# Optimization experiments

Hardware: AMD Instinct MI355X
Metric: run time of the kernel (lower is better)

## Reference

```python
import jax, jax.numpy as jnp
import numpy as np

B = 512
C = 256
HEADS = 16
DH = 16
SIGMA = 1e-4  # GaussianNoise(0.0001)
LEAK = 0.2


def _axial_attn(x, Wq, Wkv, Wo, bo, axis):
    # x: [B, 8, 4, 5, C]; attend along `axis`, folding other dims into batch.
    xm = jnp.moveaxis(x, axis, -2)                      # [..., T, C]
    q = xm @ Wq                                          # [..., T, C]
    kv = xm @ Wkv                                        # [..., T, 2C]
    k, v = kv[..., :C], kv[..., C:]
    hshape = q.shape[:-1] + (HEADS, DH)
    q = q.reshape(hshape)
    k = k.reshape(hshape)
    v = v.reshape(hshape)
    dots = jnp.einsum('...thd,...shd->...hts', q, k) * (DH ** -0.5)
    attn = jax.nn.softmax(dots, axis=-1)
    o = jnp.einsum('...hts,...shd->...thd', attn, v).reshape(xm.shape)
    o = o @ Wo + bo
    return jnp.moveaxis(o, -2, axis)


def setup_inputs() -> dict:
    key = jax.random.key(0)
    ks = jax.random.split(key, 12)
    inp = {
        'x': jax.random.normal(ks[0], (B, 8, 4, 5), jnp.float32),
        'noise': jax.random.normal(ks[1], (B, 8, 4, 5, 1), jnp.float32),
        'rand': jax.random.uniform(ks[2], (B, 8, 4, 5, 1), jnp.float32),
        # encoder Linear(2, 256, bias=False), stored as [in, out]
        'W_enc': jax.random.normal(ks[3], (2, C), jnp.float32) * (2 ** -0.5),
        # axial positional embedding (sum of per-axis params == one full param)
        'pos_emb': jax.random.normal(ks[4], (8, 4, 5, C), jnp.float32) * 0.02,
        # 2 AxialAttention layers x 3 axes of SelfAttention params
        'Wq': jax.random.normal(ks[5], (2, 3, C, C), jnp.float32) * (C ** -0.5),
        'Wkv': jax.random.normal(ks[6], (2, 3, C, 2 * C), jnp.float32) * (C ** -0.5),
        'Wo': jax.random.normal(ks[7], (2, 3, C, C), jnp.float32) * (C ** -0.5),
        'bo': jnp.zeros((2, 3, C), jnp.float32),
        # decoder Linear(256, 1, bias=True)
        'Wd': jax.random.normal(ks[8], (C, 1), jnp.float32) * (C ** -0.5),
        'bd': jnp.zeros((1,), jnp.float32),
    }
    return inp


def reference(x, noise, rand, W_enc, pos_emb, Wq, Wkv, Wo, bo, Wd, bd):
    h = x[..., None] + SIGMA * noise                  # unsqueeze + GaussianNoise
    h = jnp.concatenate([h, rand], axis=-1)           # [B,8,4,5,2]
    h = jnp.tanh(h @ W_enc)                           # [B,8,4,5,256]
    h = h + pos_emb                                   # axial positional embedding
    for l in range(2):                                # two AxialAttention blocks
        h = (_axial_attn(h, Wq[l, 0], Wkv[l, 0], Wo[l, 0], bo[l, 0], 1)
             + _axial_attn(h, Wq[l, 1], Wkv[l, 1], Wo[l, 1], bo[l, 1], 2)
             + _axial_attn(h, Wq[l, 2], Wkv[l, 2], Wo[l, 2], bo[l, 2], 3))
        h = jnp.where(h >= 0, h, LEAK * h)            # LeakyReLU(0.2)
    out = jax.nn.sigmoid(h @ Wd + bd)                 # decoder Linear + Sigmoid
    return out[..., 0]                                # squeeze(-1) -> [B,8,4,5]
```

## Files before the change

### kernel.cpp

```cpp
#include <hip/hip_runtime.h>
#include <hip/hip_bf16.h>
#include <math.h>

#define NPOS 81920
#define CDIM 256
#define SIGMA 1e-4f
#define LEAK 0.2f

typedef __hip_bfloat16 bf16;
typedef __bf16 bf16x8 __attribute__((ext_vector_type(8)));
typedef float f32x4 __attribute__((ext_vector_type(4)));

__device__ __forceinline__ float bf2f(unsigned short u) {
    return __uint_as_float(((unsigned)u) << 16);
}
__device__ __forceinline__ unsigned short f2bfu(float f) {
    bf16 h = __float2bfloat16(f);
    return *reinterpret_cast<unsigned short*>(&h);
}

__global__ void encode_kernel(const float* __restrict__ x, const float* __restrict__ noise,
                              const float* __restrict__ rnd, const float* __restrict__ We,
                              const float* __restrict__ pe, bf16* __restrict__ H) {
    int p = blockIdx.x;
    int c = threadIdx.x;
    float a = x[p] + SIGMA * noise[p];
    float b = rnd[p];
    float z = a * We[c] + b * We[CDIM + c];
    z = fminf(15.f, fmaxf(-15.f, z));
    float e = __expf(2.f * z);
    float th = 1.f - 2.f / (e + 1.f);
    H[(size_t)p * CDIM + c] = __float2bfloat16(th + pe[(p % 160) * CDIM + c]);
}

__global__ void bias3_kernel(const float* __restrict__ bo, float* __restrict__ bsum) {
    int l = blockIdx.x, c = threadIdx.x;
    bsum[l * CDIM + c] = bo[l * 768 + c] + bo[l * 768 + 256 + c] + bo[l * 768 + 512 + c];
}

__global__ void pack_qkv_kernel(const float* __restrict__ Wq, const float* __restrict__ Wkv,
                                bf16* __restrict__ out) {
    int mat = blockIdx.x / 768;
    int n = blockIdx.x % 768;
    int k = threadIdx.x;
    float v = (n < 256) ? Wq[(size_t)mat * 65536 + (size_t)k * 256 + n]
                        : Wkv[(size_t)mat * 131072 + (size_t)k * 512 + (n - 256)];
    out[(size_t)blockIdx.x * 256 + k] = __float2bfloat16(v);
}
__global__ void pack_wo_kernel(const float* __restrict__ Wo, bf16* __restrict__ out) {
    int l = blockIdx.x / 256;
    int n = blockIdx.x % 256;
    int ck = threadIdx.x;
    for (int a = 0; a < 3; a++)
        out[(size_t)(l * 256 + n) * 768 + a * 256 + ck] =
            __float2bfloat16(Wo[(((size_t)(l * 3 + a)) * 256 + ck) * 256 + n]);
}

template <int AXIS>
__device__ __forceinline__ void attn_axis(const bf16* __restrict__ QKV, bf16* __restrict__ O,
                                          int seq, int lane) {
    constexpr int T      = (AXIS == 0) ? 8 : (AXIS == 1) ? 4 : 5;
    constexpr int STRIDE = (AXIS == 0) ? 20 : (AXIS == 1) ? 5 : 1;
    int base;
    if (AXIS == 0)      { int b = seq / 20, r = seq % 20; base = b * 160 + r; }
    else if (AXIS == 1) { int b = seq / 40, r = seq % 40; base = b * 160 + (r / 5) * 20 + (r % 5); }
    else                { int b = seq / 32, r = seq % 32; base = b * 160 + r * 5; }

    float q[T][4], k[T][4], v[T][4];
#pragma unroll
    for (int t = 0; t < T; t++) {
        const unsigned short* rowp =
            (const unsigned short*)QKV + (size_t)(base + t * STRIDE) * 2304 + AXIS * 768 + lane * 4;
        ushort4 qu = *(const ushort4*)(rowp);
        ushort4 ku = *(const ushort4*)(rowp + 256);
        ushort4 vu = *(const ushort4*)(rowp + 512);
        q[t][0] = bf2f(qu.x); q[t][1] = bf2f(qu.y); q[t][2] = bf2f(qu.z); q[t][3] = bf2f(qu.w);
        k[t][0] = bf2f(ku.x); k[t][1] = bf2f(ku.y); k[t][2] = bf2f(ku.z); k[t][3] = bf2f(ku.w);
        v[t][0] = bf2f(vu.x); v[t][1] = bf2f(vu.y); v[t][2] = bf2f(vu.z); v[t][3] = bf2f(vu.w);
    }

#pragma unroll
    for (int t = 0; t < T; t++) {
        float sc[T];
#pragma unroll
        for (int s = 0; s < T; s++) {
            float p = q[t][0] * k[s][0] + q[t][1] * k[s][1] + q[t][2] * k[s][2] + q[t][3] * k[s][3];
            p += __shfl_xor(p, 1);
            p += __shfl_xor(p, 2);
            sc[s] = p * 0.25f;
        }
        float mx = sc[0];
#pragma unroll
        for (int s = 1; s < T; s++) mx = fmaxf(mx, sc[s]);
        float sum = 0.f;
#pragma unroll
        for (int s = 0; s < T; s++) { sc[s] = __expf(sc[s] - mx); sum += sc[s]; }
        float inv = 1.f / sum;
        float o0 = 0.f, o1 = 0.f, o2 = 0.f, o3 = 0.f;
#pragma unroll
        for (int s = 0; s < T; s++) {
            o0 += sc[s] * v[s][0]; o1 += sc[s] * v[s][1];
            o2 += sc[s] * v[s][2]; o3 += sc[s] * v[s][3];
        }
        ushort4 st;
        st.x = f2bfu(o0 * inv); st.y = f2bfu(o1 * inv);
        st.z = f2bfu(o2 * inv); st.w = f2bfu(o3 * inv);
        *(ushort4*)((unsigned short*)O + (size_t)(base + t * STRIDE) * 768 + AXIS * 256 + lane * 4) = st;
    }
}

__global__ __launch_bounds__(256, 2) void step_kernel(
    const bf16* __restrict__ Hg, const bf16* __restrict__ Wqkv, bf16* __restrict__ QKV,
    const bf16* __restrict__ O, const bf16* __restrict__ WoTl, bf16* __restrict__ Hnw,
    const float* __restrict__ bias,
    const bf16* __restrict__ QKVr, bf16* __restrict__ Oa,
    int nWu, int nGu, int nAu, int n0, int n1) {
    __shared__ __bf16 smem[32768];
    int tid = threadIdx.x;
    int wave = tid >> 6, lane = tid & 63;
    int quad = lane >> 4, m = lane & 15;
    int uid = blockIdx.x >> 3, l8 = blockIdx.x & 7;

    if (uid >= nWu) {
        int rem = uid - nWu;
        int tot = nGu + nAu;
        int au = rem * nAu / tot;
        bool isA = ((rem + 1) * nAu / tot) > au;
        if (isA) {
            int blk = au * 8 + l8;
            if (blk < n0)            attn_axis<0>(QKVr, Oa, blk * 4 + wave, lane);
            else if (blk < n0 + n1)  attn_axis<1>(QKVr, Oa, (blk - n0) * 4 + wave, lane);
            else                     attn_axis<2>(QKVr, Oa, (blk - n0 - n1) * 4 + wave, lane);
            return;
        }
        __bf16* As = smem;
        __bf16* Bs = smem + 8192;
        int bid = (rem - au) * 8 + l8;
        int xcd = bid & 7, slot = bid >> 3;
        int g = slot / 9;
        int nb = slot - g * 9;
        int mb = xcd + 8 * g;
        int bm = mb * 128, bn = nb * 256;
        int wr = (wave >> 1) * 64, wc = (wave & 1) * 128;
        f32x4 acc[4][8] = {};

#define STAGE_G(buf, k0)                                                                       \
    {                                                                                          \
        _Pragma("unroll") for (int rep = 0; rep < 2; rep++) {                                  \
            int ch = rep * 256 + wave * 64 + lane;                                             \
            int row = ch >> 2, cc = ch & 3, gc = cc ^ ((row >> 1) & 3);                        \
            __builtin_amdgcn_global_load_lds(                                                  \
                (const __attribute__((address_space(1))) void*)(Hg + (size_t)(bm + row) * CDIM \
                                                                + (k0) + gc * 8),              \
                (__attribute__((address_space(3))) void*)(As + (buf) * 4096                    \
                                                          + (rep * 256 + wave * 64) * 8),      \
                16, 0, 0);                                                                     \
        }                                                                                      \
        _Pragma("unroll") for (int rep = 0; rep < 4; rep++) {                                  \
            int ch = rep * 256 + wave * 64 + lane;                                             \
            int row = ch >> 2, cc = ch & 3, gc = cc ^ ((row >> 1) & 3);                        \
            __builtin_amdgcn_global_load_lds(                                                  \
                (const __attribute__((address_space(1))) void*)(Wqkv + (size_t)(bn + row) * 256\
                                                                + (k0) + gc * 8),              \
                (__attribute__((address_space(3))) void*)(Bs + (buf) * 8192                    \
                                                          + (rep * 256 + wave * 64) * 8),      \
                16, 0, 0);                                                                     \
        }                                                                                      \
    }

        STAGE_G(0, 0);
#pragma unroll
        for (int it = 0; it < 8; it++) {
            __syncthreads();
            if (it < 7) STAGE_G((it + 1) & 1, (it + 1) * 32);
            const __bf16* Ab = As + (it & 1) * 4096;
            const __bf16* Bb = Bs + (it & 1) * 8192;
            bf16x8 af[4], bfr[8];
#pragma unroll
            for (int i = 0; i < 4; i++) {
                int r = wr + i * 16 + m;
                af[i] = *(const bf16x8*)(Ab + r * 32 + ((quad ^ ((r >> 1) & 3)) * 8));
            }
#pragma unroll
            for (int j = 0; j < 8; j++) {
                int r = wc + j * 16 + m;
                bfr[j] = *(const bf16x8*)(Bb + r * 32 + ((quad ^ ((r >> 1) & 3)) * 8));
            }
#pragma unroll
            for (int i = 0; i < 4; i++)
#pragma unroll
                for (int j = 0; j < 8; j++)
                    acc[i][j] = __builtin_amdgcn_mfma_f32_16x16x32_bf16(af[i], bfr[j], acc[i][j], 0, 0, 0);
        }
#undef STAGE_G

#pragma unroll
        for (int i = 0; i < 4; i++)
#pragma unroll
            for (int j = 0; j < 8; j++)
#pragma unroll
                for (int r = 0; r < 4; r++) {
                    int row = bm + wr + i * 16 + quad * 4 + r;
                    int col = bn + wc + j * 16 + m;
                    QKV[(size_t)row * 2304 + col] = __float2bfloat16(acc[i][j][r]);
                }
    } else {
        __bf16* As = smem;
        __bf16* Bs = smem + 16384;
        int bid = blockIdx.x;
        int xcd = bid & 7, slot = bid >> 3;
        int g = slot >> 1;
        int nb = slot & 1;
        int mb = xcd + 8 * g;
        int bm = mb * 128, bn = nb * 128;
        int wr = (wave >> 1) * 64, wc = (wave & 1) * 64;
        f32x4 acc[4][4] = {};

#define STAGE_W(buf, k0)                                                                       \
    {                                                                                          \
        _Pragma("unroll") for (int rep = 0; rep < 4; rep++) {                                  \
            int ch = rep * 256 + wave * 64 + lane;                                             \
            int row = ch >> 3, cc = ch & 7, gc = cc ^ (row & 7);                               \
            __builtin_amdgcn_global_load_lds(                                                  \
                (const __attribute__((address_space(1))) void*)(O + (size_t)(bm + row) * 768   \
                                                                + (k0) + gc * 8),              \
                (__attribute__((address_space(3))) void*)(As + (buf) * 8192                    \
                                                          + (rep * 256 + wave * 64) * 8),      \
                16, 0, 0);                                                                     \
        }                                                                                      \
        _Pragma("unroll") for (int rep = 0; rep < 4; rep++) {                                  \
            int ch = rep * 256 + wave * 64 + lane;                                             \
            int row = ch >> 3, cc = ch & 7, gc = cc ^ (row & 7);                               \
            __builtin_amdgcn_global_load_lds(                                                  \
                (const __attribute__((address_space(1))) void*)(WoTl + (size_t)(bn + row) * 768\
                                                                + (k0) + gc * 8),              \
                (__attribute__((address_space(3))) void*)(Bs + (buf) * 8192                    \
                                                          + (rep * 256 + wave * 64) * 8),      \
                16, 0, 0);                                                                     \
        }                                                                                      \
    }

        STAGE_W(0, 0);
#pragma unroll
        for (int it = 0; it < 12; it++) {
            __syncthreads();
            if (it < 11) STAGE_W((it + 1) & 1, (it + 1) * 64);
            const __bf16* Ab = As + (it & 1) * 8192;
            const __bf16* Bb = Bs + (it & 1) * 8192;
#pragma unroll
            for (int kk = 0; kk < 2; kk++) {
                bf16x8 af[4], bfr[4];
#pragma unroll
                for (int i = 0; i < 4; i++) {
                    int r = wr + i * 16 + m, cix = kk * 4 + quad;
                    af[i] = *(const bf16x8*)(Ab + r * 64 + ((cix ^ (r & 7)) * 8));
                }
#pragma unroll
                for (int j = 0; j < 4; j++) {
                    int r = wc + j * 16 + m, cix = kk * 4 + quad;
                    bfr[j] = *(const bf16x8*)(Bb + r * 64 + ((cix ^ (r & 7)) * 8));
                }
#pragma unroll
                for (int i = 0; i < 4; i++)
#pragma unroll
                    for (int j = 0; j < 4; j++)
                        acc[i][j] = __builtin_amdgcn_mfma_f32_16x16x32_bf16(af[i], bfr[j], acc[i][j], 0, 0, 0);
            }
        }
#undef STAGE_W

#pragma unroll
        for (int i = 0; i < 4; i++)
#pragma unroll
            for (int j = 0; j < 4; j++)
#pragma unroll
                for (int r = 0; r < 4; r++) {
                    int row = bm + wr + i * 16 + quad * 4 + r;
                    int col = bn + wc + j * 16 + m;
                    float v = acc[i][j][r] + bias[col];
                    v = v >= 0.f ? v : LEAK * v;
                    Hnw[(size_t)row * CDIM + col] = __float2bfloat16(v);
                }
    }
}

__global__ void decode_kernel(const bf16* __restrict__ H, const float* __restrict__ Wd,
                              const float* __restrict__ bd, float* __restrict__ out) {
    int tid = threadIdx.x;
    int pos = blockIdx.x * 4 + (tid >> 6);
    int lane = tid & 63;
    float acc = 0.f;
#pragma unroll
    for (int q = 0; q < 4; q++) {
        int c = lane + q * 64;
        acc += __bfloat162float(H[(size_t)pos * CDIM + c]) * Wd[c];
    }
#pragma unroll
    for (int off = 32; off > 0; off >>= 1) acc += __shfl_down(acc, off);
    if (lane == 0) out[pos] = 1.f / (1.f + __expf(-(acc + bd[0])));
}

extern "C" void kernel_launch(void* const* d_in, const int* in_sizes, int n_in,
                              void* d_out, int out_size, void* d_ws, size_t ws_size,
                              hipStream_t stream) {
    const float* x     = (const float*)d_in[0];
    const float* noise = (const float*)d_in[1];
    const float* rnd   = (const float*)d_in[2];
    const float* We    = (const float*)d_in[3];
    const float* pe    = (const float*)d_in[4];
    const float* Wq    = (const float*)d_in[5];
    const float* Wkv   = (const float*)d_in[6];
    const float* Wo    = (const float*)d_in[7];
    const float* bo    = (const float*)d_in[8];
    const float* Wd    = (const float*)d_in[9];
    const float* bd    = (const float*)d_in[10];
    float* out = (float*)d_out;

    bf16* H0    = (bf16*)d_ws;
    bf16* H1    = H0 + (size_t)NPOS * CDIM;
    bf16* WqkvT = H1 + (size_t)NPOS * CDIM;
    bf16* WoT   = WqkvT + (size_t)2 * 2304 * 256;
    float* bsum = (float*)(WoT + (size_t)2 * 256 * 768);
    bf16* QKV0  = (bf16*)(bsum + 512);

    size_t fixed = ((size_t)2 * NPOS * CDIM + (size_t)2 * 2304 * 256 + (size_t)2 * 256 * 768) * 2
                   + 512 * 4;
    int c = 4;
    while (c < 64 && fixed + (size_t)(NPOS / c) * (2304 + 768) * 2 * 2 > ws_size) c <<= 1;
    int mc = NPOS / c;
    bf16* QKV1 = QKV0 + (size_t)mc * 2304;
    bf16* O0   = QKV1 + (size_t)mc * 2304;
    bf16* O1   = O0 + (size_t)mc * 768;
    bf16* Hbuf[3] = { H0, H1, H0 };

    pack_qkv_kernel<<<6 * 768, 256, 0, stream>>>(Wq, Wkv, WqkvT);
    pack_wo_kernel<<<2 * 256, 256, 0, stream>>>(Wo, WoT);
    bias3_kernel<<<2, 256, 0, stream>>>(bo, bsum);
    encode_kernel<<<NPOS, 256, 0, stream>>>(x, noise, rnd, We, pe, H0);

    int nMblk = mc / 128;
    int cells = mc / 160;
    int n0 = cells * 20 / 4, n1 = cells * 40 / 4, n2 = cells * 32 / 4;
    int nA = n0 + n1 + n2;
    int TT = 2 * c;

    for (int t = 0; t <= TT + 1; t++) {
        int nGu = (t < TT) ? (nMblk * 9) >> 3 : 0;
        int nAu = (t >= 1 && t <= TT) ? nA >> 3 : 0;
        int nWu = (t >= 2) ? (nMblk * 2) >> 3 : 0;

        const bf16 *HgP = nullptr, *WqP = nullptr; bf16* QKVw = nullptr;
        if (nGu) {
            int lg = t / c, cg = t % c;
            HgP  = Hbuf[lg] + (size_t)cg * mc * CDIM;
            WqP  = WqkvT + (size_t)lg * 2304 * 256;
            QKVw = (t & 1) ? QKV1 : QKV0;
        }
        const bf16* QKVr = nullptr; bf16* Oaw = nullptr;
        if (nAu) {
            int ta = t - 1;
            QKVr = (ta & 1) ? QKV1 : QKV0;
            Oaw  = (ta & 1) ? O1 : O0;
        }
        const bf16* Ord = nullptr; const bf16* WoTl = nullptr;
        bf16* Hnw = nullptr; const float* bs = nullptr;
        if (nWu) {
            int tw = t - 2, lw = tw / c, cw = tw % c;
            Ord  = (tw & 1) ? O1 : O0;
            WoTl = WoT + (size_t)lw * 256 * 768;
            Hnw  = Hbuf[lw + 1] + (size_t)cw * mc * CDIM;
            bs   = bsum + lw * CDIM;
        }
        step_kernel<<<(nWu + nGu + nAu) * 8, 256, 0, stream>>>(
            HgP, WqP, QKVw, Ord, WoTl, Hnw, bs, QKVr, Oaw, nWu, nGu, nAu, n0, n1);
    }

    decode_kernel<<<NPOS / 4, 256, 0, stream>>>(Hbuf[2], Wd, bd, out);
}
```

Measured before the change: 692.5 us.

## Shrink GEMM tiles to 128x128xK32 and raise occupancy to four blocks per CU

Both the QKV projection GEMM and the output projection GEMM now use 128x128 tiles with K-step 32 and a shared staging macro. This halves LDS use to 32 KB and raises launch bounds to 4 blocks per CU. The QKV grid doubles its N-blocks (18 per M block) to match. The attention helper also loads q per query row instead of holding every q in registers, to cut register pressure. In exchange, each output is reloaded from smaller tiles with more barriers, and operand reuse per block drops.

```diff
diff --git a/kernel.cpp b/kernel.cpp
--- a/kernel.cpp
+++ b/kernel.cpp
@@ -66,25 +66,27 @@
     else if (AXIS == 1) { int b = seq / 40, r = seq % 40; base = b * 160 + (r / 5) * 20 + (r % 5); }
     else                { int b = seq / 32, r = seq % 32; base = b * 160 + r * 5; }
 
-    float q[T][4], k[T][4], v[T][4];
+    const unsigned short* qbase =
+        (const unsigned short*)QKV + (size_t)base * 2304 + AXIS * 768 + lane * 4;
+    float k[T][4], v[T][4];
 #pragma unroll
     for (int t = 0; t < T; t++) {
-        const unsigned short* rowp =
-            (const unsigned short*)QKV + (size_t)(base + t * STRIDE) * 2304 + AXIS * 768 + lane * 4;
-        ushort4 qu = *(const ushort4*)(rowp);
+        const unsigned short* rowp = qbase + (size_t)t * STRIDE * 2304;
         ushort4 ku = *(const ushort4*)(rowp + 256);
         ushort4 vu = *(const ushort4*)(rowp + 512);
-        q[t][0] = bf2f(qu.x); q[t][1] = bf2f(qu.y); q[t][2] = bf2f(qu.z); q[t][3] = bf2f(qu.w);
         k[t][0] = bf2f(ku.x); k[t][1] = bf2f(ku.y); k[t][2] = bf2f(ku.z); k[t][3] = bf2f(ku.w);
         v[t][0] = bf2f(vu.x); v[t][1] = bf2f(vu.y); v[t][2] = bf2f(vu.z); v[t][3] = bf2f(vu.w);
     }
 
 #pragma unroll
     for (int t = 0; t < T; t++) {
+        const unsigned short* rowp = qbase + (size_t)t * STRIDE * 2304;
+        ushort4 qu = *(const ushort4*)(rowp);
+        float q0 = bf2f(qu.x), q1 = bf2f(qu.y), q2 = bf2f(qu.z), q3 = bf2f(qu.w);
         float sc[T];
 #pragma unroll
         for (int s = 0; s < T; s++) {
-            float p = q[t][0] * k[s][0] + q[t][1] * k[s][1] + q[t][2] * k[s][2] + q[t][3] * k[s][3];
+            float p = q0 * k[s][0] + q1 * k[s][1] + q2 * k[s][2] + q3 * k[s][3];
             p += __shfl_xor(p, 1);
             p += __shfl_xor(p, 2);
             sc[s] = p * 0.25f;
@@ -109,17 +111,30 @@
     }
 }
 
-__global__ __launch_bounds__(256, 2) void step_kernel(
+__global__ __launch_bounds__(256, 4) void step_kernel(
     const bf16* __restrict__ Hg, const bf16* __restrict__ Wqkv, bf16* __restrict__ QKV,
     const bf16* __restrict__ O, const bf16* __restrict__ WoTl, bf16* __restrict__ Hnw,
     const float* __restrict__ bias,
     const bf16* __restrict__ QKVr, bf16* __restrict__ Oa,
     int nWu, int nGu, int nAu, int n0, int n1) {
-    __shared__ __bf16 smem[32768];
+    __shared__ __bf16 smem[16384];
     int tid = threadIdx.x;
     int wave = tid >> 6, lane = tid & 63;
     int quad = lane >> 4, m = lane & 15;
     int uid = blockIdx.x >> 3, l8 = blockIdx.x & 7;
+
+#define STAGE_TILE(dst, src, ldk, buf, k0)                                                     \
+    {                                                                                          \
+        _Pragma("unroll") for (int rep = 0; rep < 2; rep++) {                                  \
+            int ch = rep * 256 + wave * 64 + lane;                                             \
+            int row = ch >> 2, cc = ch & 3, gc = cc ^ ((row >> 1) & 3);                        \
+            __builtin_amdgcn_global_load_lds(                                                  \
+                (const __attribute__((address_space(1))) void*)((src) + (size_t)row * (ldk)    \
+                                                                + (k0) + gc * 8),              \
+                (__attribute__((address_space(3))) void*)((dst) + (buf) * 4096 + ch * 8),      \
+                16, 0, 0);                                                                     \
+        }                                                                                      \
+    }
 
     if (uid >= nWu) {
         int rem = uid - nWu;
@@ -137,67 +152,46 @@
         __bf16* Bs = smem + 8192;
         int bid = (rem - au) * 8 + l8;
         int xcd = bid & 7, slot = bid >> 3;
-        int g = slot / 9;
-        int nb = slot - g * 9;
+        int g = slot / 18;
+        int nb = slot - g * 18;
         int mb = xcd + 8 * g;
-        int bm = mb * 128, bn = nb * 256;
-        int wr = (wave >> 1) * 64, wc = (wave & 1) * 128;
-        f32x4 acc[4][8] = {};
-
-#define STAGE_G(buf, k0)                                                                       \
-    {                                                                                          \
-        _Pragma("unroll") for (int rep = 0; rep < 2; rep++) {                                  \
-            int ch = rep * 256 + wave * 64 + lane;                                             \
-            int row = ch >> 2, cc = ch & 3, gc = cc ^ ((row >> 1) & 3);                        \
-            __builtin_amdgcn_global_load_lds(                                                  \
-                (const __attribute__((address_space(1))) void*)(Hg + (size_t)(bm + row) * CDIM \
-                                                                + (k0) + gc * 8),              \
-                (__attribute__((address_space(3))) void*)(As + (buf) * 4096                    \
-                                                          + (rep * 256 + wave * 64) * 8),      \
-                16, 0, 0);                                                                     \
-        }                                                                                      \
-        _Pragma("unroll") for (int rep = 0; rep < 4; rep++) {                                  \
-            int ch = rep * 256 + wave * 64 + lane;                                             \
-            int row = ch >> 2, cc = ch & 3, gc = cc ^ ((row >> 1) & 3);                        \
-            __builtin_amdgcn_global_load_lds(                                                  \
-                (const __attribute__((address_space(1))) void*)(Wqkv + (size_t)(bn + row) * 256\
-                                                                + (k0) + gc * 8),              \
-                (__attribute__((address_space(3))) void*)(Bs + (buf) * 8192                    \
-                                                          + (rep * 256 + wave * 64) * 8),      \
-                16, 0, 0);                                                                     \
-        }                                                                                      \
-    }
-
-        STAGE_G(0, 0);
+        int bm = mb * 128, bn = nb * 128;
+        int wr = (wave >> 1) * 64, wc = (wave & 1) * 64;
+        f32x4 acc[4][4] = {};
+
+        STAGE_TILE(As, Hg + (size_t)bm * CDIM, CDIM, 0, 0);
+        STAGE_TILE(Bs, Wqkv + (size_t)bn * 256, 256, 0, 0);
 #pragma unroll
         for (int it = 0; it < 8; it++) {
             __syncthreads();
-            if (it < 7) STAGE_G((it + 1) & 1, (it + 1) * 32);
+            if (it < 7) {
+                STAGE_TILE(As, Hg + (size_t)bm * CDIM, CDIM, (it + 1) & 1, (it + 1) * 32);
+                STAGE_TILE(Bs, Wqkv + (size_t)bn * 256, 256, (it + 1) & 1, (it + 1) * 32);
+            }
             const __bf16* Ab = As + (it & 1) * 4096;
-            const __bf16* Bb = Bs + (it & 1) * 8192;
-            bf16x8 af[4], bfr[8];
+            const __bf16* Bb = Bs + (it & 1) * 4096;
+            bf16x8 af[4], bfr[4];
 #pragma unroll
             for (int i = 0; i < 4; i++) {
                 int r = wr + i * 16 + m;
                 af[i] = *(const bf16x8*)(Ab + r * 32 + ((quad ^ ((r >> 1) & 3)) * 8));
             }
 #pragma unroll
-            for (int j = 0; j < 8; j++) {
+            for (int j = 0; j < 4; j++) {
                 int r = wc + j * 16 + m;
                 bfr[j] = *(const bf16x8*)(Bb + r * 32 + ((quad ^ ((r >> 1) & 3)) * 8));
             }
 #pragma unroll
             for (int i = 0; i < 4; i++)
 #pragma unroll
-                for (int j = 0; j < 8; j++)
+                for (int j = 0; j < 4; j++)
                     acc[i][j] = __builtin_amdgcn_mfma_f32_16x16x32_bf16(af[i], bfr[j], acc[i][j], 0, 0, 0);
         }
-#undef STAGE_G
 
 #pragma unroll
         for (int i = 0; i < 4; i++)
 #pragma unroll
-            for (int j = 0; j < 8; j++)
+            for (int j = 0; j < 4; j++)
 #pragma unroll
                 for (int r = 0; r < 4; r++) {
                     int row = bm + wr + i * 16 + quad * 4 + r;
@@ -206,7 +200,7 @@
                 }
     } else {
         __bf16* As = smem;
-        __bf16* Bs = smem + 16384;
+        __bf16* Bs = smem + 8192;
         int bid = blockIdx.x;
         int xcd = bid & 7, slot = bid >> 3;
         int g = slot >> 1;
@@ -216,58 +210,34 @@
         int wr = (wave >> 1) * 64, wc = (wave & 1) * 64;
         f32x4 acc[4][4] = {};
 
-#define STAGE_W(buf, k0)                                                                       \
-    {                                                                                          \
-        _Pragma("unroll") for (int rep = 0; rep < 4; rep++) {                                  \
-            int ch = rep * 256 + wave * 64 + lane;                                             \
-            int row = ch >> 3, cc = ch & 7, gc = cc ^ (row & 7);                               \
-            __builtin_amdgcn_global_load_lds(                                                  \
-                (const __attribute__((address_space(1))) void*)(O + (size_t)(bm + row) * 768   \
-                                                                + (k0) + gc * 8),              \
-                (__attribute__((address_space(3))) void*)(As + (buf) * 8192                    \
-                                                          + (rep * 256 + wave * 64) * 8),      \
-                16, 0, 0);                                                                     \
-        }                                                                                      \
-        _Pragma("unroll") for (int rep = 0; rep < 4; rep++) {                                  \
-            int ch = rep * 256 + wave * 64 + lane;                                             \
-            int row = ch >> 3, cc = ch & 7, gc = cc ^ (row & 7);                               \
-            __builtin_amdgcn_global_load_lds(                                                  \
-                (const __attribute__((address_space(1))) void*)(WoTl + (size_t)(bn + row) * 768\
-                                                                + (k0) + gc * 8),              \
-                (__attribute__((address_space(3))) void*)(Bs + (buf) * 8192                    \
-                                                          + (rep * 256 + wave * 64) * 8),      \
-                16, 0, 0);                                                                     \
-        }                                                                                      \
-    }
-
-        STAGE_W(0, 0);
-#pragma unroll
-        for (int it = 0; it < 12; it++) {
+        STAGE_TILE(As, O + (size_t)bm * 768, 768, 0, 0);
+        STAGE_TILE(Bs, WoTl + (size_t)bn * 768, 768, 0, 0);
+#pragma unroll
+        for (int it = 0; it < 24; it++) {
             __syncthreads();
-            if (it < 11) STAGE_W((it + 1) & 1, (it + 1) * 64);
-            const __bf16* Ab = As + (it & 1) * 8192;
-            const __bf16* Bb = Bs + (it & 1) * 8192;
-#pragma unroll
-            for (int kk = 0; kk < 2; kk++) {
-                bf16x8 af[4], bfr[4];
-#pragma unroll
-                for (int i = 0; i < 4; i++) {
-                    int r = wr + i * 16 + m, cix = kk * 4 + quad;
-                    af[i] = *(const bf16x8*)(Ab + r * 64 + ((cix ^ (r & 7)) * 8));
-                }
-#pragma unroll
-                for (int j = 0; j < 4; j++) {
-                    int r = wc + j * 16 + m, cix = kk * 4 + quad;
-                    bfr[j] = *(const bf16x8*)(Bb + r * 64 + ((cix ^ (r & 7)) * 8));
-                }
-#pragma unroll
-                for (int i = 0; i < 4; i++)
-#pragma unroll
-                    for (int j = 0; j < 4; j++)
-                        acc[i][j] = __builtin_amdgcn_mfma_f32_16x16x32_bf16(af[i], bfr[j], acc[i][j], 0, 0, 0);
-            }
-        }
-#undef STAGE_W
+            if (it < 23) {
+                STAGE_TILE(As, O + (size_t)bm * 768, 768, (it + 1) & 1, (it + 1) * 32);
+                STAGE_TILE(Bs, WoTl + (size_t)bn * 768, 768, (it + 1) & 1, (it + 1) * 32);
+            }
+            const __bf16* Ab = As + (it & 1) * 4096;
+            const __bf16* Bb = Bs + (it & 1) * 4096;
+            bf16x8 af[4], bfr[4];
+#pragma unroll
+            for (int i = 0; i < 4; i++) {
+                int r = wr + i * 16 + m;
+                af[i] = *(const bf16x8*)(Ab + r * 32 + ((quad ^ ((r >> 1) & 3)) * 8));
+            }
+#pragma unroll
+            for (int j = 0; j < 4; j++) {
+                int r = wc + j * 16 + m;
+                bfr[j] = *(const bf16x8*)(Bb + r * 32 + ((quad ^ ((r >> 1) & 3)) * 8));
+            }
+#pragma unroll
+            for (int i = 0; i < 4; i++)
+#pragma unroll
+                for (int j = 0; j < 4; j++)
+                    acc[i][j] = __builtin_amdgcn_mfma_f32_16x16x32_bf16(af[i], bfr[j], acc[i][j], 0, 0, 0);
+        }
 
 #pragma unroll
         for (int i = 0; i < 4; i++)
@@ -282,6 +252,7 @@
                     Hnw[(size_t)row * CDIM + col] = __float2bfloat16(v);
                 }
     }
+#undef STAGE_TILE
 }
 
 __global__ void decode_kernel(const bf16* __restrict__ H, const float* __restrict__ Wd,
@@ -345,7 +316,7 @@
     int TT = 2 * c;
 
     for (int t = 0; t <= TT + 1; t++) {
-        int nGu = (t < TT) ? (nMblk * 9) >> 3 : 0;
+        int nGu = (t < TT) ? (nMblk * 18) >> 3 : 0;
         int nAu = (t >= 1 && t <= TT) ? nA >> 3 : 0;
         int nWu = (t >= 2) ? (nMblk * 2) >> 3 : 0;
 
```

New measurement: 701.9 us. Within noise of the previous version (+1.4%).
